# Kernel optimization log

Measured on AMD Instinct MI355X. Metric: run time of the kernel, lower is better.

## Reference

```python
import jax, jax.numpy as jnp
import numpy as np

NUM_CODES = 8192
CODE_DIM = 512
BATCH = 32768
DECAY = 0.995
EPS = 1e-8
COMMITMENT_COST = 0.3
DIVERSITY_WEIGHT = 0.001


def setup_inputs() -> dict:
    key = jax.random.key(0)
    k1, k2, k3 = jax.random.split(key, 3)
    z = jax.random.normal(k1, (BATCH, CODE_DIM), dtype=jnp.float32)
    emb = jax.random.normal(k2, (NUM_CODES, CODE_DIM), dtype=jnp.float32)
    emb = emb / (jnp.linalg.norm(emb, axis=1, keepdims=True) + EPS)
    cluster_size = jnp.zeros((NUM_CODES,), dtype=jnp.float32)
    embed_avg = emb  # buffer initialized to embedding.clone()
    return {"z": z, "embedding": emb, "cluster_size": cluster_size, "embed_avg": embed_avg}


def reference(z, embedding, cluster_size, embed_avg):
    B, D = z.shape
    K = embedding.shape[0]

    # cosine-similarity nearest-code assignment
    z_norm = z / (jnp.linalg.norm(z, axis=1, keepdims=True) + EPS)
    emb_norm = embedding / (jnp.linalg.norm(embedding, axis=1, keepdims=True) + EPS)
    similarities = jnp.einsum('bd,kd->bk', z_norm, emb_norm)  # [B, K]
    indices = jnp.argmax(similarities, axis=1)                # [B]
    z_q = embedding[indices]                                  # gather [B, D]

    # EMA updates (training path, no_grad in torch)
    counts = jax.ops.segment_sum(jnp.ones((B,), z.dtype), indices, num_segments=K)
    new_cluster_size = DECAY * cluster_size + (1.0 - DECAY) * counts
    embed_sum = jax.ops.segment_sum(z, indices, num_segments=K)  # one_hot.T @ z
    new_embed_avg = DECAY * embed_avg + (1.0 - DECAY) * embed_sum
    n = jnp.sum(new_cluster_size)
    csn = (new_cluster_size + EPS) / (n + K * EPS) * n
    new_embedding = new_embed_avg / csn[:, None]
    new_embedding = new_embedding / (jnp.linalg.norm(new_embedding, axis=1, keepdims=True) + EPS)
    final_embed_avg = new_embedding * csn[:, None]

    # losses
    commitment_loss = jnp.mean((z - jax.lax.stop_gradient(z_q)) ** 2)
    embedding_loss = jnp.mean((jax.lax.stop_gradient(z) - z_q) ** 2)
    probs = counts / jnp.sum(counts)
    entropy = -jnp.sum(probs * jnp.log(probs + 1e-10))
    max_entropy = jnp.log(jnp.asarray(K, z.dtype))
    diversity_loss = (max_entropy - entropy) / max_entropy
    vq_loss = commitment_loss * COMMITMENT_COST + embedding_loss + DIVERSITY_WEIGHT * diversity_loss

    # straight-through output
    z_q_st = z + jax.lax.stop_gradient(z_q - z)

    # perplexity: encodings.mean(0) == counts / B
    avg_probs = counts / B
    perplexity = jnp.exp(-jnp.sum(avg_probs * jnp.log(avg_probs + 1e-10)))

    return (z_q_st, vq_loss, perplexity, indices, diversity_loss,
            new_embedding, new_cluster_size, final_embed_avg)
```

## Files before the change

kernel.cpp:

```cpp
#include <hip/hip_runtime.h>
#include <math.h>

#define BATCH 32768
#define DIM   512
#define NCODE 8192
#define DECAYF 0.995f
#define OMDF   0.005f
#define EPSF   1e-8f
#define MARGIN 8e-3f
#define MAXFLAG 2048
#define MAXTILE 12

typedef _Float16 half8 __attribute__((ext_vector_type(8)));
typedef _Float16 half4 __attribute__((ext_vector_type(4)));
typedef float f32x4 __attribute__((ext_vector_type(4)));

#define OFF_SCAL   0
#define OFF_CNT    64
#define OFF_COUNTS 128
#define OFF_ER     32896
#define OFF_IDX    65664
#define OFF_LOSS   196736
#define OFF_FROW   229504
#define OFF_NFT    237696
#define OFF_FTILE  245888
#define OFF_RVAL   344192
#define OFF_RIDX   442496
#define OFF_EH     540800
#define NLOSSBLK   4096

__device__ inline void atomAddD(double* p, double v){ unsafeAtomicAdd(p, v); }

__device__ inline void async_cp16(const _Float16* g, _Float16* l) {
  __builtin_amdgcn_global_load_lds(
      (const __attribute__((address_space(1))) unsigned int*)g,
      (__attribute__((address_space(3))) unsigned int*)l, 16, 0, 0);
}

__global__ __launch_bounds__(256) void k_prep_e(const float* __restrict__ emb,
                                                float* __restrict__ er,
                                                _Float16* __restrict__ eh) {
  int row = blockIdx.x * 4 + (threadIdx.x >> 6);
  int l = threadIdx.x & 63;
  const float4* p = (const float4*)(emb + (size_t)row * DIM);
  float4 a = p[l], b = p[l + 64];
  float s = a.x*a.x + a.y*a.y + a.z*a.z + a.w*a.w
          + b.x*b.x + b.y*b.y + b.z*b.z + b.w*b.w;
  #pragma unroll
  for (int off = 32; off > 0; off >>= 1) s += __shfl_down(s, off);
  s = __shfl(s, 0);
  float inv = 1.0f / (sqrtf(s) + EPSF);
  if (l == 0) er[row] = inv;
  half4 ha = { (_Float16)(a.x*inv), (_Float16)(a.y*inv), (_Float16)(a.z*inv), (_Float16)(a.w*inv) };
  half4 hb = { (_Float16)(b.x*inv), (_Float16)(b.y*inv), (_Float16)(b.z*inv), (_Float16)(b.w*inv) };
  *(half4*)(eh + (size_t)row * DIM + l * 4) = ha;
  *(half4*)(eh + (size_t)row * DIM + 256 + l * 4) = hb;
}

__global__ __launch_bounds__(256) void k_prep_z(const float* __restrict__ z,
                                                _Float16* __restrict__ z5,
                                                _Float16* __restrict__ z7) {
  size_t base = ((size_t)blockIdx.x * 256 + threadIdx.x) * 8;
  const float4* zp = (const float4*)(z + base);
  float4 a = zp[0], b = zp[1];
  half8 h = { (_Float16)a.x, (_Float16)a.y, (_Float16)a.z, (_Float16)a.w,
              (_Float16)b.x, (_Float16)b.y, (_Float16)b.z, (_Float16)b.w };
  _Float16* dst = (base < (size_t)16384 * 512) ? (z5 + base)
                                               : (z7 + (base - (size_t)16384 * 512));
  *(half8*)dst = h;
}

__global__ __launch_bounds__(256) void k_coarse(const _Float16* __restrict__ eh,
                                                const _Float16* __restrict__ z5,
                                                const _Float16* __restrict__ z7,
                                                float* __restrict__ c1v,
                                                float* __restrict__ c2v,
                                                int* __restrict__ c1i) {
  __shared__ _Float16 As[4096];
  __shared__ _Float16 Bs[4096];
  __shared__ float ev1[2][128];
  __shared__ float ev2[2][128];
  __shared__ int   ei1[2][128];

  const int t = threadIdx.x, w = t >> 6, lane = t & 63;
  const int quad = lane >> 4, c16 = lane & 15;
  const int row0 = blockIdx.x * 128;
  const int by = blockIdx.y, col0 = by * 128;
  const int m0 = (w & 1) * 64, n0 = (w >> 1) * 64;
  const _Float16* zbase = (row0 < 16384) ? z5 : (z7 - (size_t)16384 * 512);

  const int kq = (lane & 3) ^ ((lane >> 3) & 3);
  const _Float16* ga[2]; const _Float16* gb[2];
  _Float16* la[2]; _Float16* lb[2];
  #pragma unroll
  for (int c = 0; c < 2; c++) {
    int r = (c * 4 + w) * 16 + (lane >> 2);
    ga[c] = zbase + (size_t)(row0 + r) * 512 + kq * 8;
    gb[c] = eh + (size_t)(col0 + r) * 512 + kq * 8;
    la[c] = As + (c * 4 + w) * 512;
    lb[c] = Bs + (c * 4 + w) * 512;
  }

  f32x4 acc[4][4];
  #pragma unroll
  for (int i = 0; i < 4; i++)
    #pragma unroll
    for (int j = 0; j < 4; j++) { acc[i][j][0]=0.f; acc[i][j][1]=0.f; acc[i][j][2]=0.f; acc[i][j][3]=0.f; }

  const int sw = (c16 * 4 + (quad ^ ((c16 >> 1) & 3))) * 8;
  int offA[4], offB[4];
  #pragma unroll
  for (int i = 0; i < 4; i++) offA[i] = ((m0 >> 4) + i) * 512 + sw;
  #pragma unroll
  for (int j = 0; j < 4; j++) offB[j] = ((n0 >> 4) + j) * 512 + sw;

  for (int kk = 0; kk < 16; kk++) {
    #pragma unroll
    for (int c = 0; c < 2; c++) {
      async_cp16(ga[c], la[c]); ga[c] += 32;
      async_cp16(gb[c], lb[c]); gb[c] += 32;
    }
    __syncthreads();
    half8 af[4], bf[4];
    #pragma unroll
    for (int i = 0; i < 4; i++) af[i] = *(const half8*)(As + offA[i]);
    #pragma unroll
    for (int j = 0; j < 4; j++) bf[j] = *(const half8*)(Bs + offB[j]);
    #pragma unroll
    for (int i = 0; i < 4; i++)
      #pragma unroll
      for (int j = 0; j < 4; j++)
        acc[i][j] = __builtin_amdgcn_mfma_f32_16x16x32_f16(af[i], bf[j], acc[i][j], 0, 0, 0);
    __syncthreads();
  }

  const int h = w >> 1;
  #pragma unroll
  for (int i = 0; i < 4; i++) {
    #pragma unroll
    for (int r = 0; r < 4; r++) {
      float v1 = acc[i][0][r];
      int   i1 = col0 + n0 + c16;
      float v2 = -3.0e38f;
      #pragma unroll
      for (int j = 1; j < 4; j++) {
        float v = acc[i][j][r];
        int ix = col0 + n0 + j * 16 + c16;
        if (v > v1) { v2 = fmaxf(v2, v1); v1 = v; i1 = ix; }
        else        { v2 = fmaxf(v2, v); }
      }
      #pragma unroll
      for (int m = 1; m < 16; m <<= 1) {
        float o1 = __shfl_xor(v1, m);
        float o2 = __shfl_xor(v2, m);
        int   oi = __shfl_xor(i1, m);
        if (o1 > v1 || (o1 == v1 && oi < i1)) { v2 = fmaxf(v1, o2); v1 = o1; i1 = oi; }
        else                                  { v2 = fmaxf(v2, o1); }
      }
      if (c16 == 0) {
        int rl = (w & 1) * 64 + i * 16 + quad * 4 + r;
        ev1[h][rl] = v1; ev2[h][rl] = v2; ei1[h][rl] = i1;
      }
    }
  }
  __syncthreads();
  if (t < 128) {
    float a1 = ev1[0][t], a2 = ev2[0][t]; int ai = ei1[0][t];
    float b1 = ev1[1][t], b2 = ev2[1][t]; int bi = ei1[1][t];
    float v1, v2; int i1;
    if (b1 > a1 || (b1 == a1 && bi < ai)) { v1 = b1; i1 = bi; v2 = fmaxf(a1, b2); }
    else                                  { v1 = a1; i1 = ai; v2 = fmaxf(a2, b1); }
    size_t o = (size_t)by * BATCH + row0 + t;
    c1v[o] = v1; c2v[o] = v2; c1i[o] = i1;
  }
}

__global__ __launch_bounds__(256) void k_combine(const float* __restrict__ c1v,
                                                 const float* __restrict__ c2v,
                                                 const int* __restrict__ c1i,
                                                 int* __restrict__ idxs,
                                                 float* __restrict__ out3,
                                                 int* __restrict__ cnt,
                                                 int* __restrict__ frow,
                                                 int* __restrict__ nft,
                                                 int* __restrict__ ftile) {
  int row = blockIdx.x * 256 + threadIdx.x;
  float v1 = -3.0e38f, v2 = -3.0e38f; int i1 = 0;
  for (int ti = 0; ti < 64; ti++) {
    size_t o = (size_t)ti * BATCH + row;
    float a = c1v[o]; float a2 = c2v[o]; int ai = c1i[o];
    if (a > v1 || (a == v1 && ai < i1)) { v2 = fmaxf(v1, a2); v1 = a; i1 = ai; }
    else                                { v2 = fmaxf(v2, a); }
  }
  idxs[row] = i1;
  out3[row] = (float)i1;
  if (v1 - v2 < MARGIN) {
    int fid = atomicAdd(cnt, 1);
    if (fid < MAXFLAG) {
      frow[fid] = row;
      int jj = 0;
      for (int ti = 0; ti < 64; ti++) {
        if (c1v[(size_t)ti * BATCH + row] >= v1 - MARGIN && jj < MAXTILE)
          ftile[fid * MAXTILE + jj++] = ti;
      }
      nft[fid] = jj;
    }
  }
}

__global__ __launch_bounds__(256) void k_refine(const float* __restrict__ z,
                                                const float* __restrict__ emb,
                                                const float* __restrict__ er,
                                                const int* __restrict__ cnt,
                                                const int* __restrict__ frow,
                                                const int* __restrict__ nft,
                                                const int* __restrict__ ftile,
                                                float* __restrict__ rval,
                                                int* __restrict__ ridx) {
  __shared__ float zl[512];
  __shared__ float rv[128];
  __shared__ int   ri[128];
  int fid = blockIdx.x;
  int m = cnt[0]; if (m > MAXFLAG) m = MAXFLAG;
  if (fid >= m) return;
  int t = threadIdx.x;
  int row = frow[fid];
  if (t < 128) ((float4*)zl)[t] = *(const float4*)(z + (size_t)row * 512 + t * 4);
  __syncthreads();
  int n = nft[fid];
  for (int jj = 0; jj < n; jj++) {
    int ti = ftile[fid * MAXTILE + jj];
    if (t < 128) {
      int code = ti * 128 + t;
      const float4* ep = (const float4*)(emb + (size_t)code * 512);
      const float4* zp = (const float4*)zl;
      float a0 = 0.f, a1 = 0.f, a2 = 0.f, a3 = 0.f;
      #pragma unroll 8
      for (int d = 0; d < 128; d++) {
        float4 e4 = ep[d]; float4 z4 = zp[d];
        a0 = fmaf(e4.x, z4.x, a0); a1 = fmaf(e4.y, z4.y, a1);
        a2 = fmaf(e4.z, z4.z, a2); a3 = fmaf(e4.w, z4.w, a3);
      }
      rv[t] = ((a0 + a1) + (a2 + a3)) * er[code];
      ri[t] = code;
    }
    __syncthreads();
    for (int off = 64; off > 0; off >>= 1) {
      if (t < off) {
        if (rv[t + off] > rv[t] || (rv[t + off] == rv[t] && ri[t + off] < ri[t])) {
          rv[t] = rv[t + off]; ri[t] = ri[t + off];
        }
      }
      __syncthreads();
    }
    if (t == 0) { rval[fid * MAXTILE + jj] = rv[0]; ridx[fid * MAXTILE + jj] = ri[0]; }
    __syncthreads();
  }
}

__global__ __launch_bounds__(256) void k_merge(const int* __restrict__ cnt,
                                               const int* __restrict__ frow,
                                               const int* __restrict__ nft,
                                               const float* __restrict__ rval,
                                               const int* __restrict__ ridx,
                                               int* __restrict__ idxs,
                                               float* __restrict__ out3) {
  int fid = blockIdx.x * 256 + threadIdx.x;
  int m = cnt[0]; if (m > MAXFLAG) m = MAXFLAG;
  if (fid >= m) return;
  int n = nft[fid];
  float bv = rval[fid * MAXTILE]; int bi = ridx[fid * MAXTILE];
  for (int jj = 1; jj < n; jj++) {
    float v = rval[fid * MAXTILE + jj]; int ix = ridx[fid * MAXTILE + jj];
    if (v > bv || (v == bv && ix < bi)) { bv = v; bi = ix; }
  }
  int row = frow[fid];
  idxs[row] = bi;
  out3[row] = (float)bi;
}

__global__ __launch_bounds__(256) void k_count(const int* __restrict__ idxs,
                                               int* __restrict__ counts) {
  int row = blockIdx.x * 256 + threadIdx.x;
  atomicAdd(&counts[idxs[row]], 1);
}

__global__ __launch_bounds__(256) void k_prefix(const int* __restrict__ counts,
                                                int* __restrict__ offs,
                                                int* __restrict__ curs) {
  __shared__ int ls[256];
  int t = threadIdx.x;
  int base = t * 32;
  int local[32];
  int s = 0;
  #pragma unroll
  for (int i = 0; i < 32; i++) { local[i] = s; s += counts[base + i]; }
  ls[t] = s;
  __syncthreads();
  for (int off = 1; off < 256; off <<= 1) {
    int add = (t >= off) ? ls[t - off] : 0;
    __syncthreads();
    ls[t] += add;
    __syncthreads();
  }
  int pre = (t == 0) ? 0 : ls[t - 1];
  #pragma unroll
  for (int i = 0; i < 32; i++) {
    int o = pre + local[i];
    offs[base + i] = o;
    curs[base + i] = o;
  }
  if (t == 255) offs[NCODE] = pre + s;
}

__global__ __launch_bounds__(256) void k_bucket(const int* __restrict__ idxs,
                                                int* __restrict__ curs,
                                                int* __restrict__ bucket) {
  int row = blockIdx.x * 256 + threadIdx.x;
  int idx = idxs[row];
  int pos = atomicAdd(&curs[idx], 1);
  bucket[pos] = row;
}

__global__ __launch_bounds__(256) void k_cluster(const float* __restrict__ cs,
                                                 const int* __restrict__ counts,
                                                 float* __restrict__ out6,
                                                 double* __restrict__ scal) {
  __shared__ double s1[256], s2[256];
  int t = threadIdx.x;
  int i = blockIdx.x * 256 + t;
  float cf = (float)counts[i];
  float ncs = DECAYF * cs[i] + OMDF * cf;
  out6[i] = ncs;
  s1[t] = (double)ncs;
  s2[t] = (double)cf;
  __syncthreads();
  for (int off = 128; off > 0; off >>= 1) {
    if (t < off) { s1[t] += s1[t + off]; s2[t] += s2[t + off]; }
    __syncthreads();
  }
  if (t == 0) { atomAddD(&scal[0], s1[0]); atomAddD(&scal[1], s2[0]); }
}

__global__ __launch_bounds__(128) void k_embed(const float* __restrict__ z,
                                               const float* __restrict__ ea,
                                               const int* __restrict__ offs,
                                               const int* __restrict__ bucket,
                                               const float* __restrict__ out6,
                                               const double* __restrict__ scal,
                                               float* __restrict__ out5,
                                               float* __restrict__ out7) {
  __shared__ float red[128];
  int k = blockIdx.x;
  int t = threadIdx.x;
  int beg = offs[k], end = offs[k + 1];
  float s0 = 0.f, s1 = 0.f, s2 = 0.f, s3 = 0.f;
  for (int j = beg; j < end; j++) {
    int r = bucket[j];
    float4 zv = *(const float4*)(z + (size_t)r * 512 + t * 4);
    s0 += zv.x; s1 += zv.y; s2 += zv.z; s3 += zv.w;
  }
  float n = (float)scal[0];
  float ncs = out6[k];
  float csn = (ncs + EPSF) / (n + (float)NCODE * EPSF) * n;
  size_t base = (size_t)k * 512 + t * 4;
  float4 eav = *(const float4*)(ea + base);
  float v[4];
  v[0] = (DECAYF * eav.x + OMDF * s0) / csn;
  v[1] = (DECAYF * eav.y + OMDF * s1) / csn;
  v[2] = (DECAYF * eav.z + OMDF * s2) / csn;
  v[3] = (DECAYF * eav.w + OMDF * s3) / csn;
  float ss = v[0]*v[0] + v[1]*v[1] + v[2]*v[2] + v[3]*v[3];
  red[t] = ss;
  __syncthreads();
  for (int off = 64; off > 0; off >>= 1) {
    if (t < off) red[t] += red[t + off];
    __syncthreads();
  }
  float inv = 1.0f / (sqrtf(red[0]) + EPSF);
  #pragma unroll
  for (int j = 0; j < 4; j++) {
    float nm = v[j] * inv;
    out5[base + j] = nm;
    out7[base + j] = nm * csn;
  }
}

__global__ __launch_bounds__(256) void k_gather(
    const float* __restrict__ z, const float* __restrict__ emb,
    const int* __restrict__ idxs, float* __restrict__ out0,
    double* __restrict__ loss_part) {
  __shared__ float red[256];
  int t = threadIdx.x;
  int row = blockIdx.x * 8 + (t >> 5);
  int l = t & 31;
  int d0 = l * 16;
  int idx = idxs[row];
  const float4* zp = (const float4*)(z + (size_t)row * 512 + d0);
  const float4* ep = (const float4*)(emb + (size_t)idx * 512 + d0);
  float4* op = (float4*)(out0 + (size_t)row * 512 + d0);
  float ls = 0.f;
  #pragma unroll
  for (int q = 0; q < 4; q++) {
    float4 zv = zp[q];
    float4 ev = ep[q];
    op[q] = ev;
    float dx = zv.x - ev.x, dy = zv.y - ev.y, dz = zv.z - ev.z, dw = zv.w - ev.w;
    ls += dx*dx + dy*dy + dz*dz + dw*dw;
  }
  red[t] = ls;
  __syncthreads();
  for (int off = 128; off > 0; off >>= 1) {
    if (t < off) red[t] += red[t + off];
    __syncthreads();
  }
  if (t == 0) loss_part[blockIdx.x] = (double)red[0];
}

__global__ __launch_bounds__(256) void k_scalars(const int* __restrict__ counts,
                                                 const double* __restrict__ scal,
                                                 const double* __restrict__ loss_part,
                                                 float* __restrict__ out1,
                                                 float* __restrict__ out2,
                                                 float* __restrict__ out4) {
  __shared__ double r1[256], r2[256], r3[256];
  int t = threadIdx.x;
  double csum = scal[1];
  double e1 = 0.0, e2 = 0.0, lsum = 0.0;
  for (int i = t; i < NCODE; i += 256) {
    double c = (double)counts[i];
    double p = c / csum;
    e1 += p * log(p + 1e-10);
    double a = c / (double)BATCH;
    e2 += a * log(a + 1e-10);
  }
  for (int i = t; i < NLOSSBLK; i += 256) lsum += loss_part[i];
  r1[t] = e1; r2[t] = e2; r3[t] = lsum;
  __syncthreads();
  for (int off = 128; off > 0; off >>= 1) {
    if (t < off) { r1[t] += r1[t+off]; r2[t] += r2[t+off]; r3[t] += r3[t+off]; }
    __syncthreads();
  }
  if (t == 0) {
    double entropy = -r1[0];
    double maxent = log((double)NCODE);
    double div = (maxent - entropy) / maxent;
    double mse = r3[0] / ((double)BATCH * (double)DIM);
    double vq = 0.3 * mse + mse + 0.001 * div;
    double perp = exp(-r2[0]);
    *out1 = (float)vq;
    *out2 = (float)perp;
    *out4 = (float)div;
  }
}

extern "C" void kernel_launch(void* const* d_in, const int* in_sizes, int n_in,
                              void* d_out, int out_size, void* d_ws, size_t ws_size,
                              hipStream_t stream) {
  const float* z   = (const float*)d_in[0];
  const float* emb = (const float*)d_in[1];
  const float* cs  = (const float*)d_in[2];
  const float* ea  = (const float*)d_in[3];

  float* out  = (float*)d_out;
  float* out0 = out;
  float* out1 = out + 16777216;
  float* out2 = out + 16777217;
  float* out3 = out + 16777218;
  float* out4 = out + 16809986;
  float* out5 = out + 16809987;
  float* out6 = out + 21004291;
  float* out7 = out + 21012483;

  char* ws = (char*)d_ws;
  double* scal      = (double*)(ws + OFF_SCAL);
  int*    cnt       = (int*)   (ws + OFF_CNT);
  int*    counts    = (int*)   (ws + OFF_COUNTS);
  float*  er        = (float*) (ws + OFF_ER);
  int*    idxs      = (int*)   (ws + OFF_IDX);
  double* loss_part = (double*)(ws + OFF_LOSS);
  int*    frow      = (int*)   (ws + OFF_FROW);
  int*    nft       = (int*)   (ws + OFF_NFT);
  int*    ftile     = (int*)   (ws + OFF_FTILE);
  float*  rval      = (float*) (ws + OFF_RVAL);
  int*    ridx      = (int*)   (ws + OFF_RIDX);
  _Float16* eh      = (_Float16*)(ws + OFF_EH);

  _Float16* zh5 = (_Float16*)out5;
  _Float16* zh7 = (_Float16*)out7;
  float* c1v = out0;
  float* c2v = out0 + (size_t)64 * BATCH;
  int*   c1i = (int*)(out0 + (size_t)128 * BATCH);
  int*   offs   = (int*)(out0 + 13500000);
  int*   curs   = offs + NCODE + 64;
  int*   bucket = curs + NCODE;

  hipMemsetAsync(ws, 0, OFF_ER, stream);

  k_prep_e<<<NCODE / 4, 256, 0, stream>>>(emb, er, eh);
  k_prep_z<<<8192, 256, 0, stream>>>(z, zh5, zh7);
  k_coarse<<<dim3(BATCH / 128, NCODE / 128), 256, 0, stream>>>(eh, zh5, zh7, c1v, c2v, c1i);
  k_combine<<<BATCH / 256, 256, 0, stream>>>(c1v, c2v, c1i, idxs, out3, cnt, frow, nft, ftile);
  k_refine<<<MAXFLAG, 256, 0, stream>>>(z, emb, er, cnt, frow, nft, ftile, rval, ridx);
  k_merge<<<MAXFLAG / 256, 256, 0, stream>>>(cnt, frow, nft, rval, ridx, idxs, out3);

  k_count<<<BATCH / 256, 256, 0, stream>>>(idxs, counts);
  k_cluster<<<NCODE / 256, 256, 0, stream>>>(cs, counts, out6, scal);
  k_prefix<<<1, 256, 0, stream>>>(counts, offs, curs);
  k_bucket<<<BATCH / 256, 256, 0, stream>>>(idxs, curs, bucket);
  k_embed<<<NCODE, 128, 0, stream>>>(z, ea, offs, bucket, out6, scal, out5, out7);

  k_gather<<<NLOSSBLK, 256, 0, stream>>>(z, emb, idxs, out0, loss_part);
  k_scalars<<<1, 256, 0, stream>>>(counts, scal, loss_part, out1, out2, out4);
}
```

Measured before the change: 853.4 us.

## Enlarge coarse GEMM tile to 256x256 with double-buffered async LDS pipeline

Rewrites the fp16 MFMA similarity kernel to use 256x256 output tiles with 512 threads, a K-step of 64, and double-buffered LDS staging. The next tile is prefetched while the current one computes, with explicit waitcnt, barriers and setprio around the MFMA phases. Each wave holds 8x4 accumulators. Larger tiles halve the number of column tiles, so the combine and refine stages now handle 32 tiles of 256 codes each. This cuts global/LDS traffic per FLOP and sync overhead, at the cost of higher register and LDS pressure (64KB LDS) and possibly more codes rescanned per flagged row in refine.

```diff
diff --git a/kernel.cpp b/kernel.cpp
--- a/kernel.cpp
+++ b/kernel.cpp
@@ -10,6 +10,8 @@
 #define MARGIN 8e-3f
 #define MAXFLAG 2048
 #define MAXTILE 12
+#define NCTILE 32
+#define NKT 8
 
 typedef _Float16 half8 __attribute__((ext_vector_type(8)));
 typedef _Float16 half4 __attribute__((ext_vector_type(4)));
@@ -70,82 +72,119 @@
   *(half8*)dst = h;
 }
 
-__global__ __launch_bounds__(256) void k_coarse(const _Float16* __restrict__ eh,
-                                                const _Float16* __restrict__ z5,
-                                                const _Float16* __restrict__ z7,
-                                                float* __restrict__ c1v,
-                                                float* __restrict__ c2v,
-                                                int* __restrict__ c1i) {
-  __shared__ _Float16 As[4096];
-  __shared__ _Float16 Bs[4096];
-  __shared__ float ev1[2][128];
-  __shared__ float ev2[2][128];
-  __shared__ int   ei1[2][128];
-
-  const int t = threadIdx.x, w = t >> 6, lane = t & 63;
-  const int quad = lane >> 4, c16 = lane & 15;
-  const int row0 = blockIdx.x * 128;
-  const int by = blockIdx.y, col0 = by * 128;
-  const int m0 = (w & 1) * 64, n0 = (w >> 1) * 64;
+__global__ __launch_bounds__(512, 2) void k_coarse(const _Float16* __restrict__ eh,
+                                                   const _Float16* __restrict__ z5,
+                                                   const _Float16* __restrict__ z7,
+                                                   float* __restrict__ c1v,
+                                                   float* __restrict__ c2v,
+                                                   int* __restrict__ c1i) {
+  __shared__ alignas(16) _Float16 As[2][16384];
+  __shared__ alignas(16) _Float16 Bs[2][16384];
+
+  const int t = threadIdx.x;
+  const int w = t >> 6, lane = t & 63;
+  const int wr = w >> 2, wc = w & 3;
+  const int c16 = lane & 15, quad = lane >> 4;
+  const int row0 = blockIdx.x * 256;
+  const int col0 = blockIdx.y * 256;
   const _Float16* zbase = (row0 < 16384) ? z5 : (z7 - (size_t)16384 * 512);
 
-  const int kq = (lane & 3) ^ ((lane >> 3) & 3);
-  const _Float16* ga[2]; const _Float16* gb[2];
-  _Float16* la[2]; _Float16* lb[2];
-  #pragma unroll
-  for (int c = 0; c < 2; c++) {
-    int r = (c * 4 + w) * 16 + (lane >> 2);
-    ga[c] = zbase + (size_t)(row0 + r) * 512 + kq * 8;
-    gb[c] = eh + (size_t)(col0 + r) * 512 + kq * 8;
-    la[c] = As + (c * 4 + w) * 512;
-    lb[c] = Bs + (c * 4 + w) * 512;
-  }
-
-  f32x4 acc[4][4];
-  #pragma unroll
-  for (int i = 0; i < 4; i++)
+  const int lr = lane >> 3;
+  const int ks = (lane & 7) ^ lr;
+  const _Float16* gA0 = zbase + (size_t)(row0 + 8 * w + lr) * 512 + ks * 8;
+  const _Float16* gB0 = eh    + (size_t)(col0 + 8 * w + lr) * 512 + ks * 8;
+
+#define STAGE(KT, B_) do {                                                  \
+    const _Float16* ga_ = gA0 + (KT) * 64;                                  \
+    const _Float16* gb_ = gB0 + (KT) * 64;                                  \
+    _Float16* la_ = &As[(B_)][512 * w];                                     \
+    _Float16* lb_ = &Bs[(B_)][512 * w];                                     \
+    _Pragma("unroll")                                                       \
+    for (int i_ = 0; i_ < 4; i_++) {                                        \
+      async_cp16(ga_ + (size_t)(64 * i_) * 512, la_ + 4096 * i_);           \
+      async_cp16(gb_ + (size_t)(64 * i_) * 512, lb_ + 4096 * i_);           \
+    }                                                                       \
+  } while (0)
+
+  f32x4 acc[8][4];
+  #pragma unroll
+  for (int i = 0; i < 8; i++)
     #pragma unroll
     for (int j = 0; j < 4; j++) { acc[i][j][0]=0.f; acc[i][j][1]=0.f; acc[i][j][2]=0.f; acc[i][j][3]=0.f; }
 
-  const int sw = (c16 * 4 + (quad ^ ((c16 >> 1) & 3))) * 8;
-  int offA[4], offB[4];
-  #pragma unroll
-  for (int i = 0; i < 4; i++) offA[i] = ((m0 >> 4) + i) * 512 + sw;
-  #pragma unroll
-  for (int j = 0; j < 4; j++) offB[j] = ((n0 >> 4) + j) * 512 + sw;
-
-  for (int kk = 0; kk < 16; kk++) {
-    #pragma unroll
-    for (int c = 0; c < 2; c++) {
-      async_cp16(ga[c], la[c]); ga[c] += 32;
-      async_cp16(gb[c], lb[c]); gb[c] += 32;
+  const int sq = c16 & 7;
+  const int colh0 = ((0 + quad) ^ sq) * 8;
+  const int colh1 = ((4 + quad) ^ sq) * 8;
+  const int arow = (wr * 128 + c16) * 64;
+  const int brow = (wc * 64 + c16) * 64;
+
+#define MM(MG, MI, N_, AF, BF)                                              \
+  acc[(MG)*4+(MI)][(N_)] =                                                  \
+      __builtin_amdgcn_mfma_f32_16x16x32_f16((AF), (BF), acc[(MG)*4+(MI)][(N_)], 0, 0, 0)
+
+#define PHASE(Ab, Bb, MG, COLH) do {                                        \
+    const _Float16* ap_ = (Ab) + arow + (MG) * 4096 + (COLH);               \
+    const _Float16* bp_ = (Bb) + brow + (COLH);                             \
+    half8 af0 = *(const half8*)(ap_);                                       \
+    half8 af1 = *(const half8*)(ap_ + 1024);                                \
+    half8 af2 = *(const half8*)(ap_ + 2048);                                \
+    half8 af3 = *(const half8*)(ap_ + 3072);                                \
+    half8 bf0 = *(const half8*)(bp_);                                       \
+    half8 bf1 = *(const half8*)(bp_ + 1024);                                \
+    half8 bf2 = *(const half8*)(bp_ + 2048);                                \
+    half8 bf3 = *(const half8*)(bp_ + 3072);                                \
+    asm volatile("" ::: "memory");                                          \
+    __builtin_amdgcn_s_barrier();                                           \
+    asm volatile("s_waitcnt lgkmcnt(0)" ::: "memory");                      \
+    __builtin_amdgcn_sched_barrier(0);                                      \
+    __builtin_amdgcn_s_setprio(1);                                          \
+    MM(MG,0,0,af0,bf0); MM(MG,0,1,af0,bf1); MM(MG,0,2,af0,bf2); MM(MG,0,3,af0,bf3); \
+    MM(MG,1,0,af1,bf0); MM(MG,1,1,af1,bf1); MM(MG,1,2,af1,bf2); MM(MG,1,3,af1,bf3); \
+    MM(MG,2,0,af2,bf0); MM(MG,2,1,af2,bf1); MM(MG,2,2,af2,bf2); MM(MG,2,3,af2,bf3); \
+    MM(MG,3,0,af3,bf0); MM(MG,3,1,af3,bf1); MM(MG,3,2,af3,bf2); MM(MG,3,3,af3,bf3); \
+    __builtin_amdgcn_s_setprio(0);                                          \
+    asm volatile("" ::: "memory");                                          \
+    __builtin_amdgcn_s_barrier();                                           \
+  } while (0)
+
+  STAGE(0, 0);
+  for (int j = 0; j < NKT; j++) {
+    const int b = j & 1;
+    if (j + 1 < NKT) {
+      STAGE(j + 1, b ^ 1);
+      asm volatile("s_waitcnt vmcnt(8)" ::: "memory");
+    } else {
+      asm volatile("s_waitcnt vmcnt(0)" ::: "memory");
     }
-    __syncthreads();
-    half8 af[4], bf[4];
-    #pragma unroll
-    for (int i = 0; i < 4; i++) af[i] = *(const half8*)(As + offA[i]);
-    #pragma unroll
-    for (int j = 0; j < 4; j++) bf[j] = *(const half8*)(Bs + offB[j]);
-    #pragma unroll
-    for (int i = 0; i < 4; i++)
-      #pragma unroll
-      for (int j = 0; j < 4; j++)
-        acc[i][j] = __builtin_amdgcn_mfma_f32_16x16x32_f16(af[i], bf[j], acc[i][j], 0, 0, 0);
-    __syncthreads();
-  }
-
-  const int h = w >> 1;
-  #pragma unroll
-  for (int i = 0; i < 4; i++) {
+    __builtin_amdgcn_s_barrier();
+    asm volatile("" ::: "memory");
+    const _Float16* Ab = As[b];
+    const _Float16* Bb = Bs[b];
+    PHASE(Ab, Bb, 0, colh0);
+    PHASE(Ab, Bb, 1, colh0);
+    PHASE(Ab, Bb, 0, colh1);
+    PHASE(Ab, Bb, 1, colh1);
+  }
+#undef PHASE
+#undef MM
+#undef STAGE
+
+  float* ev1 = (float*)&As[0][0];
+  float* ev2 = ev1 + 1024;
+  int*   ei1 = (int*)(ev2 + 1024);
+  asm volatile("" ::: "memory");
+
+  #pragma unroll
+  for (int am = 0; am < 8; am++) {
     #pragma unroll
     for (int r = 0; r < 4; r++) {
-      float v1 = acc[i][0][r];
-      int   i1 = col0 + n0 + c16;
+      float v1 = acc[am][0][r];
+      int   i1 = col0 + wc * 64 + c16;
       float v2 = -3.0e38f;
       #pragma unroll
-      for (int j = 1; j < 4; j++) {
-        float v = acc[i][j][r];
-        int ix = col0 + n0 + j * 16 + c16;
+      for (int n = 1; n < 4; n++) {
+        float v = acc[am][n][r];
+        int ix = col0 + wc * 64 + n * 16 + c16;
         if (v > v1) { v2 = fmaxf(v2, v1); v1 = v; i1 = ix; }
         else        { v2 = fmaxf(v2, v); }
       }
@@ -158,19 +197,21 @@
         else                                  { v2 = fmaxf(v2, o1); }
       }
       if (c16 == 0) {
-        int rl = (w & 1) * 64 + i * 16 + quad * 4 + r;
-        ev1[h][rl] = v1; ev2[h][rl] = v2; ei1[h][rl] = i1;
+        int rl = wr * 128 + (am >> 2) * 64 + (am & 3) * 16 + quad * 4 + r;
+        ev1[wc * 256 + rl] = v1; ev2[wc * 256 + rl] = v2; ei1[wc * 256 + rl] = i1;
       }
     }
   }
   __syncthreads();
-  if (t < 128) {
-    float a1 = ev1[0][t], a2 = ev2[0][t]; int ai = ei1[0][t];
-    float b1 = ev1[1][t], b2 = ev2[1][t]; int bi = ei1[1][t];
-    float v1, v2; int i1;
-    if (b1 > a1 || (b1 == a1 && bi < ai)) { v1 = b1; i1 = bi; v2 = fmaxf(a1, b2); }
-    else                                  { v1 = a1; i1 = ai; v2 = fmaxf(a2, b1); }
-    size_t o = (size_t)by * BATCH + row0 + t;
+  if (t < 256) {
+    float v1 = ev1[t], v2 = ev2[t]; int i1 = ei1[t];
+    #pragma unroll
+    for (int q = 1; q < 4; q++) {
+      float b1 = ev1[q * 256 + t], b2 = ev2[q * 256 + t]; int bi = ei1[q * 256 + t];
+      if (b1 > v1 || (b1 == v1 && bi < i1)) { v2 = fmaxf(v1, b2); v1 = b1; i1 = bi; }
+      else                                  { v2 = fmaxf(v2, b1); }
+    }
+    size_t o = (size_t)blockIdx.y * BATCH + row0 + t;
     c1v[o] = v1; c2v[o] = v2; c1i[o] = i1;
   }
 }
@@ -186,7 +227,7 @@
                                                  int* __restrict__ ftile) {
   int row = blockIdx.x * 256 + threadIdx.x;
   float v1 = -3.0e38f, v2 = -3.0e38f; int i1 = 0;
-  for (int ti = 0; ti < 64; ti++) {
+  for (int ti = 0; ti < NCTILE; ti++) {
     size_t o = (size_t)ti * BATCH + row;
     float a = c1v[o]; float a2 = c2v[o]; int ai = c1i[o];
     if (a > v1 || (a == v1 && ai < i1)) { v2 = fmaxf(v1, a2); v1 = a; i1 = ai; }
@@ -199,7 +240,7 @@
     if (fid < MAXFLAG) {
       frow[fid] = row;
       int jj = 0;
-      for (int ti = 0; ti < 64; ti++) {
+      for (int ti = 0; ti < NCTILE; ti++) {
         if (c1v[(size_t)ti * BATCH + row] >= v1 - MARGIN && jj < MAXTILE)
           ftile[fid * MAXTILE + jj++] = ti;
       }
@@ -218,8 +259,8 @@
                                                 float* __restrict__ rval,
                                                 int* __restrict__ ridx) {
   __shared__ float zl[512];
-  __shared__ float rv[128];
-  __shared__ int   ri[128];
+  __shared__ float rv[256];
+  __shared__ int   ri[256];
   int fid = blockIdx.x;
   int m = cnt[0]; if (m > MAXFLAG) m = MAXFLAG;
   if (fid >= m) return;
@@ -230,22 +271,20 @@
   int n = nft[fid];
   for (int jj = 0; jj < n; jj++) {
     int ti = ftile[fid * MAXTILE + jj];
-    if (t < 128) {
-      int code = ti * 128 + t;
-      const float4* ep = (const float4*)(emb + (size_t)code * 512);
-      const float4* zp = (const float4*)zl;
-      float a0 = 0.f, a1 = 0.f, a2 = 0.f, a3 = 0.f;
-      #pragma unroll 8
-      for (int d = 0; d < 128; d++) {
-        float4 e4 = ep[d]; float4 z4 = zp[d];
-        a0 = fmaf(e4.x, z4.x, a0); a1 = fmaf(e4.y, z4.y, a1);
-        a2 = fmaf(e4.z, z4.z, a2); a3 = fmaf(e4.w, z4.w, a3);
-      }
-      rv[t] = ((a0 + a1) + (a2 + a3)) * er[code];
-      ri[t] = code;
+    int code = ti * 256 + t;
+    const float4* ep = (const float4*)(emb + (size_t)code * 512);
+    const float4* zp = (const float4*)zl;
+    float a0 = 0.f, a1 = 0.f, a2 = 0.f, a3 = 0.f;
+    #pragma unroll 8
+    for (int d = 0; d < 128; d++) {
+      float4 e4 = ep[d]; float4 z4 = zp[d];
+      a0 = fmaf(e4.x, z4.x, a0); a1 = fmaf(e4.y, z4.y, a1);
+      a2 = fmaf(e4.z, z4.z, a2); a3 = fmaf(e4.w, z4.w, a3);
     }
-    __syncthreads();
-    for (int off = 64; off > 0; off >>= 1) {
+    rv[t] = ((a0 + a1) + (a2 + a3)) * er[code];
+    ri[t] = code;
+    __syncthreads();
+    for (int off = 128; off > 0; off >>= 1) {
       if (t < off) {
         if (rv[t + off] > rv[t] || (rv[t + off] == rv[t] && ri[t + off] < ri[t])) {
           rv[t] = rv[t + off]; ri[t] = ri[t + off];
@@ -489,8 +528,8 @@
   _Float16* zh5 = (_Float16*)out5;
   _Float16* zh7 = (_Float16*)out7;
   float* c1v = out0;
-  float* c2v = out0 + (size_t)64 * BATCH;
-  int*   c1i = (int*)(out0 + (size_t)128 * BATCH);
+  float* c2v = out0 + (size_t)NCTILE * BATCH;
+  int*   c1i = (int*)(out0 + (size_t)2 * NCTILE * BATCH);
   int*   offs   = (int*)(out0 + 13500000);
   int*   curs   = offs + NCODE + 64;
   int*   bucket = curs + NCODE;
@@ -499,7 +538,7 @@
 
   k_prep_e<<<NCODE / 4, 256, 0, stream>>>(emb, er, eh);
   k_prep_z<<<8192, 256, 0, stream>>>(z, zh5, zh7);
-  k_coarse<<<dim3(BATCH / 128, NCODE / 128), 256, 0, stream>>>(eh, zh5, zh7, c1v, c2v, c1i);
+  k_coarse<<<dim3(BATCH / 256, NCODE / 256), 512, 0, stream>>>(eh, zh5, zh7, c1v, c2v, c1i);
   k_combine<<<BATCH / 256, 256, 0, stream>>>(c1v, c2v, c1i, idxs, out3, cnt, frow, nft, ftile);
   k_refine<<<MAXFLAG, 256, 0, stream>>>(z, emb, er, cnt, frow, nft, ftile, rval, ridx);
   k_merge<<<MAXFLAG / 256, 256, 0, stream>>>(cnt, frow, nft, rval, ridx, idxs, out3);
```

After: 1.012 ms. 18.6% more time.

## Load coarse GEMM fragments directly from global into registers, dropping LDS staging

Applied to the files above, without the earlier changes.

The coarse fp16 similarity GEMM no longer stages A/B tiles through shared memory with async global-to-LDS copies and barriers. Each lane now loads its MFMA fragments straight from global memory into registers, double-buffered across k-steps, and the loop is fully unrolled. This removes the per-iteration __syncthreads and LDS traffic. In exchange, operand reuse across waves now relies on L1/L2 hits, and each lane issues strided 16-byte loads across rows, which may be less coalesced.

```diff
diff --git a/kernel.cpp b/kernel.cpp
--- a/kernel.cpp
+++ b/kernel.cpp
@@ -31,12 +31,6 @@
 
 __device__ inline void atomAddD(double* p, double v){ unsafeAtomicAdd(p, v); }
 
-__device__ inline void async_cp16(const _Float16* g, _Float16* l) {
-  __builtin_amdgcn_global_load_lds(
-      (const __attribute__((address_space(1))) unsigned int*)g,
-      (__attribute__((address_space(3))) unsigned int*)l, 16, 0, 0);
-}
-
 __global__ __launch_bounds__(256) void k_prep_e(const float* __restrict__ emb,
                                                 float* __restrict__ er,
                                                 _Float16* __restrict__ eh) {
@@ -76,8 +70,6 @@
                                                 float* __restrict__ c1v,
                                                 float* __restrict__ c2v,
                                                 int* __restrict__ c1i) {
-  __shared__ _Float16 As[4096];
-  __shared__ _Float16 Bs[4096];
   __shared__ float ev1[2][128];
   __shared__ float ev2[2][128];
   __shared__ int   ei1[2][128];
@@ -89,16 +81,11 @@
   const int m0 = (w & 1) * 64, n0 = (w >> 1) * 64;
   const _Float16* zbase = (row0 < 16384) ? z5 : (z7 - (size_t)16384 * 512);
 
-  const int kq = (lane & 3) ^ ((lane >> 3) & 3);
-  const _Float16* ga[2]; const _Float16* gb[2];
-  _Float16* la[2]; _Float16* lb[2];
-  #pragma unroll
-  for (int c = 0; c < 2; c++) {
-    int r = (c * 4 + w) * 16 + (lane >> 2);
-    ga[c] = zbase + (size_t)(row0 + r) * 512 + kq * 8;
-    gb[c] = eh + (size_t)(col0 + r) * 512 + kq * 8;
-    la[c] = As + (c * 4 + w) * 512;
-    lb[c] = Bs + (c * 4 + w) * 512;
+  const _Float16* ap[4]; const _Float16* bp[4];
+  #pragma unroll
+  for (int i = 0; i < 4; i++) {
+    ap[i] = zbase + (size_t)(row0 + m0 + i * 16 + c16) * 512 + quad * 8;
+    bp[i] = eh    + (size_t)(col0 + n0 + i * 16 + c16) * 512 + quad * 8;
   }
 
   f32x4 acc[4][4];
@@ -107,31 +94,34 @@
     #pragma unroll
     for (int j = 0; j < 4; j++) { acc[i][j][0]=0.f; acc[i][j][1]=0.f; acc[i][j][2]=0.f; acc[i][j][3]=0.f; }
 
-  const int sw = (c16 * 4 + (quad ^ ((c16 >> 1) & 3))) * 8;
-  int offA[4], offB[4];
-  #pragma unroll
-  for (int i = 0; i < 4; i++) offA[i] = ((m0 >> 4) + i) * 512 + sw;
-  #pragma unroll
-  for (int j = 0; j < 4; j++) offB[j] = ((n0 >> 4) + j) * 512 + sw;
-
-  for (int kk = 0; kk < 16; kk++) {
+  half8 a0[4], b0[4], a1[4], b1[4];
+  #pragma unroll
+  for (int i = 0; i < 4; i++) { a0[i] = *(const half8*)(ap[i]); b0[i] = *(const half8*)(bp[i]); }
+
+  #pragma unroll
+  for (int kk = 0; kk < 16; kk += 2) {
     #pragma unroll
-    for (int c = 0; c < 2; c++) {
-      async_cp16(ga[c], la[c]); ga[c] += 32;
-      async_cp16(gb[c], lb[c]); gb[c] += 32;
+    for (int i = 0; i < 4; i++) {
+      a1[i] = *(const half8*)(ap[i] + (kk + 1) * 32);
+      b1[i] = *(const half8*)(bp[i] + (kk + 1) * 32);
     }
-    __syncthreads();
-    half8 af[4], bf[4];
-    #pragma unroll
-    for (int i = 0; i < 4; i++) af[i] = *(const half8*)(As + offA[i]);
-    #pragma unroll
-    for (int j = 0; j < 4; j++) bf[j] = *(const half8*)(Bs + offB[j]);
     #pragma unroll
     for (int i = 0; i < 4; i++)
       #pragma unroll
       for (int j = 0; j < 4; j++)
-        acc[i][j] = __builtin_amdgcn_mfma_f32_16x16x32_f16(af[i], bf[j], acc[i][j], 0, 0, 0);
-    __syncthreads();
+        acc[i][j] = __builtin_amdgcn_mfma_f32_16x16x32_f16(a0[i], b0[j], acc[i][j], 0, 0, 0);
+    if (kk + 2 < 16) {
+      #pragma unroll
+      for (int i = 0; i < 4; i++) {
+        a0[i] = *(const half8*)(ap[i] + (kk + 2) * 32);
+        b0[i] = *(const half8*)(bp[i] + (kk + 2) * 32);
+      }
+    }
+    #pragma unroll
+    for (int i = 0; i < 4; i++)
+      #pragma unroll
+      for (int j = 0; j < 4; j++)
+        acc[i][j] = __builtin_amdgcn_mfma_f32_16x16x32_f16(a1[i], b1[j], acc[i][j], 0, 0, 0);
   }
 
   const int h = w >> 1;
@@ -165,11 +155,11 @@
   }
   __syncthreads();
   if (t < 128) {
-    float a1 = ev1[0][t], a2 = ev2[0][t]; int ai = ei1[0][t];
-    float b1 = ev1[1][t], b2 = ev2[1][t]; int bi = ei1[1][t];
+    float a1v = ev1[0][t], a2v = ev2[0][t]; int ai = ei1[0][t];
+    float b1v = ev1[1][t], b2v = ev2[1][t]; int bi = ei1[1][t];
     float v1, v2; int i1;
-    if (b1 > a1 || (b1 == a1 && bi < ai)) { v1 = b1; i1 = bi; v2 = fmaxf(a1, b2); }
-    else                                  { v1 = a1; i1 = ai; v2 = fmaxf(a2, b1); }
+    if (b1v > a1v || (b1v == a1v && bi < ai)) { v1 = b1v; i1 = bi; v2 = fmaxf(a1v, b2v); }
+    else                                      { v1 = a1v; i1 = ai; v2 = fmaxf(a2v, b1v); }
     size_t o = (size_t)by * BATCH + row0 + t;
     c1v[o] = v1; c2v[o] = v2; c1i[o] = i1;
   }
```

New measurement: 1.353 ms. 1.59x slower.
